# Kernel optimization log

Hardware: AMD Instinct MI355X
Metric: run time of the kernel (lower is better)

## Reference

```python
import jax, jax.numpy as jnp
import numpy as np

B, S, DIM, HEADS, DHEAD = 1, 1992, 2048, 16, 128
NKI_SEQ_ALIGN = 128
EPS = 1e-6


def setup_inputs() -> dict:
    key = jax.random.key(0)
    ks = jax.random.split(key, 8)
    hidden_states = jax.random.normal(ks[0], (B, S, DIM), dtype=jnp.float32)
    # realistic rotary tables, full head_dim with interleaved pair angles
    pos = jnp.arange(S, dtype=jnp.float32)
    inv_freq = 1.0 / (10000.0 ** (jnp.arange(0, DHEAD, 2, dtype=jnp.float32) / DHEAD))
    ang = pos[:, None] * inv_freq[None, :]                      # [S, DHEAD/2]
    full = jnp.stack([ang, ang], axis=-1).reshape(S, DHEAD)     # interleave
    freqs_cos = jnp.cos(full)[None, :, None, :]                 # [1,S,1,DHEAD]
    freqs_sin = jnp.sin(full)[None, :, None, :]
    sc = 0.02
    wq = jax.random.normal(ks[1], (DIM, DIM), dtype=jnp.float32) * sc
    wk = jax.random.normal(ks[2], (DIM, DIM), dtype=jnp.float32) * sc
    wv = jax.random.normal(ks[3], (DIM, DIM), dtype=jnp.float32) * sc
    wo = jax.random.normal(ks[4], (DIM, DIM), dtype=jnp.float32) * sc
    bq = jax.random.normal(ks[5], (DIM,), dtype=jnp.float32) * sc
    bk = jax.random.normal(ks[6], (DIM,), dtype=jnp.float32) * sc
    bv = jax.random.normal(ks[7], (DIM,), dtype=jnp.float32) * sc
    bo = jnp.zeros((DIM,), dtype=jnp.float32)
    norm_q_w = jnp.ones((DIM,), dtype=jnp.float32)
    norm_k_w = jnp.ones((DIM,), dtype=jnp.float32)
    return dict(hidden_states=hidden_states, freqs_cos=freqs_cos, freqs_sin=freqs_sin,
                wq=wq, bq=bq, wk=wk, bk=bk, wv=wv, bv=bv,
                norm_q_w=norm_q_w, norm_k_w=norm_k_w, wo=wo, bo=bo)


def _rms_norm(x, weight, eps=EPS):
    xf = x.astype(jnp.float32)
    var = jnp.mean(xf * xf, axis=-1, keepdims=True)
    return (weight * (xf * jax.lax.rsqrt(var + eps))).astype(x.dtype)


def _apply_rope(x, freqs_cos, freqs_sin):
    # x: [B,H,S,D]; freqs: [1,S,1,D]
    cos = jnp.transpose(freqs_cos[..., 0::2], (0, 2, 1, 3))  # [1,1,S,D/2]
    sin = jnp.transpose(freqs_sin[..., 1::2], (0, 2, 1, 3))
    x1, x2 = x[..., 0::2], x[..., 1::2]
    o1 = x1 * cos - x2 * sin
    o2 = x1 * sin + x2 * cos
    return jnp.stack([o1, o2], axis=-1).reshape(x.shape)


def _attention_padded(q, k, v):
    # Faithful to nki_flash_attention: zero-pad seq to multiple of 128,
    # no masking of padded keys (they contribute logit 0), trim query pad.
    B_, H_, S_, D_ = q.shape
    pad = (-S_) % NKI_SEQ_ALIGN
    if pad:
        pc = [(0, 0), (0, 0), (0, pad), (0, 0)]
        q = jnp.pad(q, pc); k = jnp.pad(k, pc); v = jnp.pad(v, pc)
    scale = 1.0 / np.sqrt(D_)
    scores = jnp.einsum('bhqd,bhkd->bhqk', q, k) * scale
    probs = jax.nn.softmax(scores, axis=-1)
    out = jnp.einsum('bhqk,bhkd->bhqd', probs, v)
    return out[:, :, :S_, :]


def reference(hidden_states, freqs_cos, freqs_sin, wq, bq, wk, bk, wv, bv,
              norm_q_w, norm_k_w, wo, bo):
    b, s, _ = hidden_states.shape
    q = hidden_states @ wq.T + bq
    k = hidden_states @ wk.T + bk
    v = hidden_states @ wv.T + bv
    q = _rms_norm(q, norm_q_w)
    k = _rms_norm(k, norm_k_w)
    hd = q.shape[-1] // HEADS
    q = q.reshape(b, s, HEADS, hd).transpose(0, 2, 1, 3)
    k = k.reshape(b, s, HEADS, hd).transpose(0, 2, 1, 3)
    v = v.reshape(b, s, HEADS, hd).transpose(0, 2, 1, 3)
    q = _apply_rope(q, freqs_cos, freqs_sin)
    k = _apply_rope(k, freqs_cos, freqs_sin)
    o = _attention_padded(q, k, v)
    o = o.transpose(0, 2, 1, 3).reshape(b, s, -1)
    return o @ wo.T + bo
```

## Files before the change

### kernel.cpp

```cpp
#include <hip/hip_runtime.h>
#include <cstdint>

#define S_REAL 1992
#define S_PAD  2048
#define DIMSZ  2048
#define NHEAD  16
#define DHD    128

typedef float f32x4 __attribute__((ext_vector_type(4)));
typedef float f32x16 __attribute__((ext_vector_type(16)));
typedef __bf16 bf16x8 __attribute__((ext_vector_type(8)));
typedef unsigned short u16x8 __attribute__((ext_vector_type(8)));

__device__ __forceinline__ unsigned short f2bf(float f){
  uint32_t u = __float_as_uint(f);
  u += 0x7fffu + ((u >> 16) & 1u);
  return (unsigned short)(u >> 16);
}

__device__ __forceinline__ void gload16(const void* g, void* l){
  __builtin_amdgcn_global_load_lds(
      (const __attribute__((address_space(1))) uint32_t*)g,
      (__attribute__((address_space(3))) uint32_t*)l,
      16, 0, 0);
}

template<int N> __device__ __forceinline__ void waitbar(){
  if constexpr (N == 4) asm volatile("s_waitcnt vmcnt(4)\n\ts_barrier" ::: "memory");
  else                  asm volatile("s_waitcnt vmcnt(0)\n\ts_barrier" ::: "memory");
}

__launch_bounds__(256)
__global__ void k_cvt5(const float* __restrict__ s0, const float* __restrict__ s1,
                       const float* __restrict__ s2, const float* __restrict__ s3,
                       const float* __restrict__ s4,
                       unsigned short* __restrict__ d0, unsigned short* __restrict__ d1,
                       unsigned short* __restrict__ d2, unsigned short* __restrict__ d3,
                       unsigned short* __restrict__ d4,
                       int nX, int nW)
{
  int i = blockIdx.x * 256 + threadIdx.x;
  const float* s; unsigned short* d; int j;
  if (i < nX){ s = s0; d = d0; j = i; }
  else {
    int k = i - nX;
    int wsel = k / nW; j = k - wsel * nW;
    s = (wsel == 0) ? s1 : (wsel == 1) ? s2 : (wsel == 2) ? s3 : s4;
    d = (wsel == 0) ? d1 : (wsel == 1) ? d2 : (wsel == 2) ? d3 : d4;
  }
  const float4* sp = (const float4*)s + (size_t)j * 2;
  float4 a = sp[0], b = sp[1];
  u16x8 o;
  o[0]=f2bf(a.x); o[1]=f2bf(a.y); o[2]=f2bf(a.z); o[3]=f2bf(a.w);
  o[4]=f2bf(b.x); o[5]=f2bf(b.y); o[6]=f2bf(b.z); o[7]=f2bf(b.w);
  *((u16x8*)d + j) = o;
}

__launch_bounds__(256, 3)
__global__ void k_g32(const unsigned short* __restrict__ A,
                      const unsigned short* __restrict__ B0,
                      const unsigned short* __restrict__ B1,
                      const unsigned short* __restrict__ B2,
                      const float* __restrict__ bias0,
                      const float* __restrict__ bias1,
                      const float* __restrict__ bias2,
                      float* __restrict__ C0, float* __restrict__ C1,
                      unsigned short* __restrict__ Cb,
                      int Mreal)
{
  constexpr int BUFE = 8192;
  constexpr int NT   = DIMSZ / 32;
  __shared__ unsigned short lds[3 * BUFE];

  const unsigned short* Bm = (blockIdx.z == 0) ? B0 : ((blockIdx.z == 1) ? B1 : B2);
  const float* bias        = (blockIdx.z == 0) ? bias0 : ((blockIdx.z == 1) ? bias1 : bias2);
  float* C                 = (blockIdx.z == 0) ? C0 : C1;

  const int fid = blockIdx.x + gridDim.x * blockIdx.y;
  const int q   = (gridDim.x * gridDim.y) >> 3;
  const int nf  = (fid & 7) * q + (fid >> 3);
  const int m0  = (nf >> 4) * 128, n0 = (nf & 15) * 128;

  const int tid = threadIdx.x;
  const int w = tid >> 6, l = tid & 63;
  const int l31 = l & 31, l5 = l >> 5;
  const int wr = (w >> 1) * 64, wc = (w & 1) * 64;

  f32x16 acc[2][2];
  #pragma unroll
  for (int mb = 0; mb < 2; ++mb)
    #pragma unroll
    for (int nb = 0; nb < 2; ++nb)
      #pragma unroll
      for (int r = 0; r < 16; ++r) acc[mb][nb][r] = 0.f;

#define G32_STAGE(TT, BASE) do{                                                   \
    const int k0s = (TT) * 32;                                                    \
    unsigned short* dst = (BASE);                                                 \
    _Pragma("unroll")                                                             \
    for (int i_ = 0; i_ < 2; ++i_){                                               \
      int lin = i_ * 256 + tid;                                                   \
      int r_ = lin >> 2, pos_ = lin & 3;                                          \
      int gr_ = m0 + r_; if (gr_ > Mreal - 1) gr_ = Mreal - 1;                    \
      gload16(A + (size_t)gr_ * DIMSZ + k0s + (pos_ ^ ((r_ >> 1) & 3)) * 8,       \
              dst + lin * 8);                                                     \
    }                                                                             \
    _Pragma("unroll")                                                             \
    for (int i_ = 0; i_ < 2; ++i_){                                               \
      int lin = i_ * 256 + tid;                                                   \
      int r_ = lin >> 2, pos_ = lin & 3;                                          \
      gload16(Bm + (size_t)(n0 + r_) * DIMSZ + k0s + (pos_ ^ ((r_ >> 1) & 3)) * 8,\
              dst + 4096 + lin * 8);                                              \
    }                                                                             \
  } while(0)

#define G32_COMPUTE(BASE) do{                                                     \
    const unsigned short* sb = (BASE);                                            \
    bf16x8 a_[2][2], b_[2][2];                                                    \
    _Pragma("unroll")                                                             \
    for (int mb = 0; mb < 2; ++mb)                                                \
      _Pragma("unroll")                                                           \
      for (int ks = 0; ks < 2; ++ks){                                             \
        int r_ = wr + mb * 32 + l31;                                              \
        int c_ = (ks * 2 + l5) ^ ((r_ >> 1) & 3);                                 \
        a_[mb][ks] = *(const bf16x8*)(sb + r_ * 32 + c_ * 8);                     \
      }                                                                           \
    _Pragma("unroll")                                                             \
    for (int nb = 0; nb < 2; ++nb)                                                \
      _Pragma("unroll")                                                           \
      for (int ks = 0; ks < 2; ++ks){                                             \
        int r_ = wc + nb * 32 + l31;                                              \
        int c_ = (ks * 2 + l5) ^ ((r_ >> 1) & 3);                                 \
        b_[nb][ks] = *(const bf16x8*)(sb + 4096 + r_ * 32 + c_ * 8);              \
      }                                                                           \
    __builtin_amdgcn_s_setprio(1);                                                \
    _Pragma("unroll")                                                             \
    for (int ks = 0; ks < 2; ++ks)                                                \
      _Pragma("unroll")                                                           \
      for (int mb = 0; mb < 2; ++mb)                                              \
        _Pragma("unroll")                                                         \
        for (int nb = 0; nb < 2; ++nb)                                            \
          acc[mb][nb] = __builtin_amdgcn_mfma_f32_32x32x16_bf16(a_[mb][ks],       \
                            b_[nb][ks], acc[mb][nb], 0, 0, 0);                    \
    __builtin_amdgcn_s_setprio(0);                                                \
  } while(0)

  G32_STAGE(0, lds);
  G32_STAGE(1, lds + BUFE);
  int bc = 0, bs = 2;
  for (int tt = 0; tt < NT - 2; ++tt){
    waitbar<4>();
    G32_STAGE(tt + 2, lds + bs * BUFE);
    G32_COMPUTE(lds + bc * BUFE);
    bs = (bs == 2) ? 0 : bs + 1;
    bc = (bc == 2) ? 0 : bc + 1;
  }
  waitbar<4>();
  G32_COMPUTE(lds + bc * BUFE);
  bc = (bc == 2) ? 0 : bc + 1;
  waitbar<0>();
  G32_COMPUTE(lds + bc * BUFE);

#undef G32_STAGE
#undef G32_COMPUTE

  const bool vout = (blockIdx.z == 2);
  #pragma unroll
  for (int nb = 0; nb < 2; ++nb){
    int col = n0 + wc + nb * 32 + l31;
    float bz = bias[col];
    #pragma unroll
    for (int mb = 0; mb < 2; ++mb){
      #pragma unroll
      for (int r = 0; r < 16; ++r){
        int row = m0 + wr + mb * 32 + (r & 3) + 8 * (r >> 2) + 4 * l5;
        if (row < Mreal){
          if (vout) Cb[(size_t)row * DIMSZ + col] = f2bf(acc[mb][nb][r] + bz);
          else      C[(size_t)row * DIMSZ + col] = acc[mb][nb][r] + bz;
        }
      }
    }
  }
}

__launch_bounds__(256)
__global__ void k_normrope2(const float* __restrict__ Qf, const float* __restrict__ Kf,
                            const float* __restrict__ nqw, const float* __restrict__ nkw,
                            const float* __restrict__ fc, const float* __restrict__ fs,
                            unsigned short* __restrict__ OutQ, unsigned short* __restrict__ OutK)
{
  const int s = blockIdx.x;
  const int isK = blockIdx.y;
  const float* Xf = isK ? Kf : Qf;
  const float* nw = isK ? nkw : nqw;
  unsigned short* Out = isK ? OutK : OutQ;
  const float scale = isK ? 1.0f : 0.08838834764831843f;
  const int swz = isK;

  const int t = threadIdx.x;
  const int w = t >> 6, l = t & 63;
  __shared__ float wred[4];
  float v[8];
  float ss = 0.f;
  if (s < S_REAL){
    const float4* p = (const float4*)(Xf + (size_t)s * DIMSZ) + t * 2;
    float4 a = p[0], b = p[1];
    v[0]=a.x; v[1]=a.y; v[2]=a.z; v[3]=a.w; v[4]=b.x; v[5]=b.y; v[6]=b.z; v[7]=b.w;
    #pragma unroll
    for (int j = 0; j < 8; ++j) ss += v[j] * v[j];
  }
  #pragma unroll
  for (int off = 32; off >= 1; off >>= 1) ss += __shfl_xor(ss, off);
  if (l == 0) wred[w] = ss;
  __syncthreads();
  float tot = wred[0] + wred[1] + wred[2] + wred[3];
  float rinv = rsqrtf(tot * (1.f / DIMSZ) + 1e-6f);

  const int h  = t >> 4;
  const int d0 = (t & 15) * 8;
  const int b  = t & 15;
  const int bsw = swz ? (b ^ (s & 7)) : b;
  unsigned short* dst = Out + ((size_t)h * S_PAD + s) * DHD + bsw * 8;
  u16x8 o;
  if (s < S_REAL){
    #pragma unroll
    for (int i = 0; i < 4; ++i){
      float c_ = fc[s * DHD + d0 + 2 * i];
      float s_ = fs[s * DHD + d0 + 2 * i + 1];
      float x1 = v[2 * i]     * rinv * nw[t * 8 + 2 * i];
      float x2 = v[2 * i + 1] * rinv * nw[t * 8 + 2 * i + 1];
      o[2 * i]     = f2bf((x1 * c_ - x2 * s_) * scale);
      o[2 * i + 1] = f2bf((x1 * s_ + x2 * c_) * scale);
    }
  } else {
    #pragma unroll
    for (int j = 0; j < 8; ++j) o[j] = 0;
  }
  *(u16x8*)dst = o;
}

__launch_bounds__(256)
__global__ void k_vtrans(const unsigned short* __restrict__ Vb, unsigned short* __restrict__ Vth)
{
  __shared__ unsigned short tile[64][72];
  const int t = threadIdx.x;
  const int s0 = blockIdx.x * 64, c0 = blockIdx.y * 64;
  #pragma unroll
  for (int i = 0; i < 2; ++i){
    int lin = i * 256 + t;
    int r = lin >> 3, ck = lin & 7;
    u16x8 val = (u16x8){0,0,0,0,0,0,0,0};
    if (s0 + r < S_REAL)
      val = *(const u16x8*)(Vb + (size_t)(s0 + r) * DIMSZ + c0 + ck * 8);
    *(u16x8*)&tile[r][ck * 8] = val;
  }
  __syncthreads();
  const int cl = t >> 2;
  const int cc = c0 + cl;
  #pragma unroll
  for (int bi = 0; bi < 2; ++bi){
    int b = (t & 3) * 2 + bi;
    u16x8 o;
    #pragma unroll
    for (int j = 0; j < 8; ++j) o[j] = tile[b * 8 + j][cl];
    int bsw = b ^ (cc & 7);
    *(u16x8*)(Vth + (size_t)cc * S_PAD + s0 + bsw * 8) = o;
  }
}

__launch_bounds__(512)
__global__ void k_attn(const unsigned short* __restrict__ Qh,
                       const unsigned short* __restrict__ Kh,
                       const unsigned short* __restrict__ Vth,
                       unsigned short* __restrict__ O)
{
  __shared__ unsigned short kbuf[3][64 * 128];
  __shared__ unsigned short vbuf[3][128 * 64];
  __shared__ unsigned short pbuf[8][16 * 64];
  const int h = blockIdx.y;
  const int q0 = blockIdx.x * 128;
  const int t = threadIdx.x, w = t >> 6, l = t & 63;
  const int lr = l & 15, lg = l >> 4;

  const unsigned short* Qp = Qh + ((size_t)h * S_PAD + q0 + w * 16 + lr) * DHD;
  bf16x8 qf[4];
  #pragma unroll
  for (int ks = 0; ks < 4; ++ks) qf[ks] = *(const bf16x8*)(Qp + ks * 32 + lg * 8);

  f32x4 acc[8];
  #pragma unroll
  for (int nf = 0; nf < 8; ++nf) acc[nf] = (f32x4){0.f, 0.f, 0.f, 0.f};
  float m = -3.0e38f, lsum = 0.f;

#define ATT_STAGE(KT, BI) do{                                                       \
    _Pragma("unroll")                                                               \
    for (int i_ = 0; i_ < 2; ++i_){                                                 \
      int lin = i_ * 512 + t;                                                       \
      int rK = lin >> 4, ckK = lin & 15;                                            \
      gload16(Kh + ((size_t)h * S_PAD + (KT) * 64 + rK) * DHD + ckK * 8,            \
              &kbuf[BI][lin * 8]);                                                  \
    }                                                                               \
    _Pragma("unroll")                                                               \
    for (int i_ = 0; i_ < 2; ++i_){                                                 \
      int lin = i_ * 512 + t;                                                       \
      int rV = lin >> 3, ckV = lin & 7;                                             \
      gload16(Vth + ((size_t)h * DHD + rV) * S_PAD + (KT) * 64 + ckV * 8,           \
              &vbuf[BI][lin * 8]);                                                  \
    }                                                                               \
  } while(0)

  ATT_STAGE(0, 0);
  ATT_STAGE(1, 1);
  asm volatile("s_waitcnt vmcnt(4)" ::: "memory");
  __builtin_amdgcn_s_barrier();

  constexpr int NKT = S_PAD / 64;
  for (int kt = 0; kt < NKT; ++kt){
    const int bi = kt % 3;
    if (kt < NKT - 2) ATT_STAGE(kt + 2, (kt + 2) % 3);

    f32x4 sf[4];
    __builtin_amdgcn_s_setprio(1);
    #pragma unroll
    for (int kvf = 0; kvf < 4; ++kvf){
      sf[kvf] = (f32x4){0.f, 0.f, 0.f, 0.f};
      int r = kvf * 16 + lr;
      #pragma unroll
      for (int ks = 0; ks < 4; ++ks){
        int blk = (ks * 4 + lg) ^ (r & 7);
        bf16x8 kf = *(const bf16x8*)&kbuf[bi][r * 128 + blk * 8];
        sf[kvf] = __builtin_amdgcn_mfma_f32_16x16x32_bf16(kf, qf[ks], sf[kvf], 0, 0, 0);
      }
    }
    __builtin_amdgcn_s_setprio(0);

    float pmax = sf[0][0];
    #pragma unroll
    for (int kvf = 0; kvf < 4; ++kvf)
      #pragma unroll
      for (int j = 0; j < 4; ++j) pmax = fmaxf(pmax, sf[kvf][j]);
    pmax = fmaxf(pmax, __shfl_xor(pmax, 16));
    pmax = fmaxf(pmax, __shfl_xor(pmax, 32));

    float fr = 1.f;
    if (!__all(pmax - m <= 8.0f)){
      float mn = fmaxf(m, pmax);
      fr = __expf(m - mn);
      m = mn;
      float fv0 = __shfl(fr, lg * 4 + 0);
      float fv1 = __shfl(fr, lg * 4 + 1);
      float fv2 = __shfl(fr, lg * 4 + 2);
      float fv3 = __shfl(fr, lg * 4 + 3);
      f32x4 fv = (f32x4){fv0, fv1, fv2, fv3};
      #pragma unroll
      for (int nf = 0; nf < 8; ++nf) acc[nf] *= fv;
    }

    float p[4][4];
    float psum = 0.f;
    #pragma unroll
    for (int kvf = 0; kvf < 4; ++kvf)
      #pragma unroll
      for (int j = 0; j < 4; ++j){ p[kvf][j] = __expf(sf[kvf][j] - m); psum += p[kvf][j]; }
    lsum = lsum * fr + psum;

    char* pb = (char*)pbuf[w];
    #pragma unroll
    for (int kvf = 0; kvf < 4; ++kvf){
      uint2 wv;
      wv.x = (uint32_t)f2bf(p[kvf][0]) | ((uint32_t)f2bf(p[kvf][1]) << 16);
      wv.y = (uint32_t)f2bf(p[kvf][2]) | ((uint32_t)f2bf(p[kvf][3]) << 16);
      int byte = lr * 128 + (((kvf * 2 + (lg >> 1)) ^ (lr & 7)) * 16) + (lg & 1) * 8;
      *(uint2*)(pb + byte) = wv;
    }
    bf16x8 pf[2];
    #pragma unroll
    for (int c = 0; c < 2; ++c)
      pf[c] = *(const bf16x8*)(pb + lr * 128 + ((c * 4 + lg) ^ (lr & 7)) * 16);

    __builtin_amdgcn_s_setprio(1);
    #pragma unroll
    for (int nf = 0; nf < 8; ++nf){
      int cc = nf * 16 + lr;
      #pragma unroll
      for (int ks = 0; ks < 2; ++ks){
        int blk = (ks * 4 + lg) ^ (cc & 7);
        bf16x8 vf = *(const bf16x8*)&vbuf[bi][cc * 64 + blk * 8];
        acc[nf] = __builtin_amdgcn_mfma_f32_16x16x32_bf16(pf[ks], vf, acc[nf], 0, 0, 0);
      }
    }
    __builtin_amdgcn_s_setprio(0);

    if (kt < NKT - 2)       asm volatile("s_waitcnt vmcnt(4)" ::: "memory");
    else if (kt == NKT - 2) asm volatile("s_waitcnt vmcnt(0)" ::: "memory");
    if (kt < NKT - 1) __builtin_amdgcn_s_barrier();
  }
#undef ATT_STAGE

  lsum += __shfl_xor(lsum, 16);
  lsum += __shfl_xor(lsum, 32);
  float ls0 = __shfl(lsum, lg * 4 + 0);
  float ls1 = __shfl(lsum, lg * 4 + 1);
  float ls2 = __shfl(lsum, lg * 4 + 2);
  float ls3 = __shfl(lsum, lg * 4 + 3);
  f32x4 lsv = (f32x4){1.f / ls0, 1.f / ls1, 1.f / ls2, 1.f / ls3};

  #pragma unroll
  for (int nf = 0; nf < 8; ++nf){
    #pragma unroll
    for (int j = 0; j < 4; ++j){
      int row = q0 + w * 16 + lg * 4 + j;
      if (row < S_REAL)
        O[(size_t)row * DIMSZ + h * DHD + nf * 16 + lr] = f2bf(acc[nf][j] * lsv[j]);
    }
  }
}

extern "C" void kernel_launch(void* const* d_in, const int* in_sizes, int n_in,
                              void* d_out, int out_size, void* d_ws, size_t ws_size,
                              hipStream_t stream)
{
  const float* hidden = (const float*)d_in[0];
  const float* fc  = (const float*)d_in[1];
  const float* fs  = (const float*)d_in[2];
  const float* wq  = (const float*)d_in[3];
  const float* bq  = (const float*)d_in[4];
  const float* wk  = (const float*)d_in[5];
  const float* bk  = (const float*)d_in[6];
  const float* wv  = (const float*)d_in[7];
  const float* bv  = (const float*)d_in[8];
  const float* nqw = (const float*)d_in[9];
  const float* nkw = (const float*)d_in[10];
  const float* wo  = (const float*)d_in[11];
  const float* bo  = (const float*)d_in[12];
  float* out = (float*)d_out;

  char* ws = (char*)d_ws;
  size_t off = 0;
  auto alloc = [&](size_t bytes) -> void* {
    void* p = ws + off;
    off += (bytes + 255) & ~(size_t)255;
    return p;
  };
  unsigned short* Xb  = (unsigned short*)alloc((size_t)S_REAL * DIMSZ * 2);
  unsigned short* Wqb = (unsigned short*)alloc((size_t)DIMSZ * DIMSZ * 2);
  unsigned short* Wkb = (unsigned short*)alloc((size_t)DIMSZ * DIMSZ * 2);
  unsigned short* Wvb = (unsigned short*)alloc((size_t)DIMSZ * DIMSZ * 2);
  unsigned short* Wob = (unsigned short*)alloc((size_t)DIMSZ * DIMSZ * 2);
  float* Qf = (float*)alloc((size_t)S_REAL * DIMSZ * 4);
  float* Kf = (float*)alloc((size_t)S_REAL * DIMSZ * 4);
  unsigned short* Vb  = (unsigned short*)alloc((size_t)S_REAL * DIMSZ * 2);
  unsigned short* Qhh = (unsigned short*)alloc((size_t)NHEAD * S_PAD * DHD * 2);
  unsigned short* Khh = (unsigned short*)alloc((size_t)NHEAD * S_PAD * DHD * 2);
  unsigned short* Vth = (unsigned short*)alloc((size_t)NHEAD * DHD * S_PAD * 2);
  unsigned short* Oa  = (unsigned short*)alloc((size_t)S_REAL * DIMSZ * 2);

  {
    int nX = S_REAL * DIMSZ / 8;
    int nW = DIMSZ * DIMSZ / 8;
    int total = nX + 4 * nW;
    k_cvt5<<<total / 256, 256, 0, stream>>>(hidden, wq, wk, wv, wo,
                                            Xb, Wqb, Wkb, Wvb, Wob, nX, nW);
  }

  k_g32<<<dim3(16, 16, 3), 256, 0, stream>>>(Xb, Wqb, Wkb, Wvb, bq, bk, bv,
                                             Qf, Kf, Vb, S_REAL);

  k_normrope2<<<dim3(S_PAD, 2), 256, 0, stream>>>(Qf, Kf, nqw, nkw, fc, fs, Qhh, Khh);

  k_vtrans<<<dim3(S_PAD / 64, DIMSZ / 64), 256, 0, stream>>>(Vb, Vth);

  k_attn<<<dim3(S_PAD / 128, NHEAD), 512, 0, stream>>>(Qhh, Khh, Vth, Oa);

  k_g32<<<dim3(16, 16, 1), 256, 0, stream>>>(Oa, Wob, Wob, Wob, bo, bo, bo,
                                             out, out, nullptr, S_REAL);
}
```

Measured before the change: 221.2 us.

## Deepen GEMM K-tile, software-pipeline attention softmax, use exp2 and head swizzle

```diff
diff --git a/kernel.cpp b/kernel.cpp
--- a/kernel.cpp
+++ b/kernel.cpp
@@ -23,11 +23,6 @@
       (const __attribute__((address_space(1))) uint32_t*)g,
       (__attribute__((address_space(3))) uint32_t*)l,
       16, 0, 0);
-}
-
-template<int N> __device__ __forceinline__ void waitbar(){
-  if constexpr (N == 4) asm volatile("s_waitcnt vmcnt(4)\n\ts_barrier" ::: "memory");
-  else                  asm volatile("s_waitcnt vmcnt(0)\n\ts_barrier" ::: "memory");
 }
 
 __launch_bounds__(256)
@@ -56,8 +51,9 @@
   *((u16x8*)d + j) = o;
 }
 
-__launch_bounds__(256, 3)
-__global__ void k_g32(const unsigned short* __restrict__ A,
+template<int BN>
+__launch_bounds__(256, 2)
+__global__ void k_g64(const unsigned short* __restrict__ A,
                       const unsigned short* __restrict__ B0,
                       const unsigned short* __restrict__ B1,
                       const unsigned short* __restrict__ B2,
@@ -68,9 +64,16 @@
                       unsigned short* __restrict__ Cb,
                       int Mreal)
 {
-  constexpr int BUFE = 8192;
-  constexpr int NT   = DIMSZ / 32;
-  __shared__ unsigned short lds[3 * BUFE];
+  constexpr int WN   = (BN == 128) ? 2 : 1;
+  constexpr int WM   = 4 / WN;
+  constexpr int MB   = (128 / WM) / 32;
+  constexpr int NB   = (BN / WN) / 32;
+  constexpr int AE   = 128 * 64;
+  constexpr int BE   = BN * 64;
+  constexpr int BUFE = AE + BE;
+  constexpr int NT   = DIMSZ / 64;
+  constexpr int TN   = DIMSZ / BN;
+  __shared__ unsigned short lds[2 * BUFE];
 
   const unsigned short* Bm = (blockIdx.z == 0) ? B0 : ((blockIdx.z == 1) ? B1 : B2);
   const float* bias        = (blockIdx.z == 0) ? bias0 : ((blockIdx.z == 1) ? bias1 : bias2);
@@ -79,98 +82,94 @@
   const int fid = blockIdx.x + gridDim.x * blockIdx.y;
   const int q   = (gridDim.x * gridDim.y) >> 3;
   const int nf  = (fid & 7) * q + (fid >> 3);
-  const int m0  = (nf >> 4) * 128, n0 = (nf & 15) * 128;
+  const int m0  = (nf / TN) * 128, n0 = (nf % TN) * BN;
 
   const int tid = threadIdx.x;
   const int w = tid >> 6, l = tid & 63;
   const int l31 = l & 31, l5 = l >> 5;
-  const int wr = (w >> 1) * 64, wc = (w & 1) * 64;
-
-  f32x16 acc[2][2];
-  #pragma unroll
-  for (int mb = 0; mb < 2; ++mb)
-    #pragma unroll
-    for (int nb = 0; nb < 2; ++nb)
+  const int wr = (w / WN) * (128 / WM);
+  const int wc = (w % WN) * (BN / WN);
+
+  f32x16 acc[MB][NB];
+  #pragma unroll
+  for (int mb = 0; mb < MB; ++mb)
+    #pragma unroll
+    for (int nb = 0; nb < NB; ++nb)
       #pragma unroll
       for (int r = 0; r < 16; ++r) acc[mb][nb][r] = 0.f;
 
-#define G32_STAGE(TT, BASE) do{                                                   \
-    const int k0s = (TT) * 32;                                                    \
-    unsigned short* dst = (BASE);                                                 \
+#define G64_STAGE(TT, PP) do{                                                     \
+    const int k0s = (TT) * 64;                                                    \
+    unsigned short* dst = &lds[(PP) * BUFE];                                      \
     _Pragma("unroll")                                                             \
-    for (int i_ = 0; i_ < 2; ++i_){                                               \
+    for (int i_ = 0; i_ < AE / 2048; ++i_){                                       \
       int lin = i_ * 256 + tid;                                                   \
-      int r_ = lin >> 2, pos_ = lin & 3;                                          \
+      int r_ = lin >> 3, sl_ = lin & 7;                                           \
       int gr_ = m0 + r_; if (gr_ > Mreal - 1) gr_ = Mreal - 1;                    \
-      gload16(A + (size_t)gr_ * DIMSZ + k0s + (pos_ ^ ((r_ >> 1) & 3)) * 8,       \
+      gload16(A + (size_t)gr_ * DIMSZ + k0s + (sl_ ^ (r_ & 7)) * 8,               \
               dst + lin * 8);                                                     \
     }                                                                             \
     _Pragma("unroll")                                                             \
-    for (int i_ = 0; i_ < 2; ++i_){                                               \
+    for (int i_ = 0; i_ < BE / 2048; ++i_){                                       \
       int lin = i_ * 256 + tid;                                                   \
-      int r_ = lin >> 2, pos_ = lin & 3;                                          \
-      gload16(Bm + (size_t)(n0 + r_) * DIMSZ + k0s + (pos_ ^ ((r_ >> 1) & 3)) * 8,\
-              dst + 4096 + lin * 8);                                              \
+      int r_ = lin >> 3, sl_ = lin & 7;                                           \
+      gload16(Bm + (size_t)(n0 + r_) * DIMSZ + k0s + (sl_ ^ (r_ & 7)) * 8,        \
+              dst + AE + lin * 8);                                                \
     }                                                                             \
   } while(0)
 
-#define G32_COMPUTE(BASE) do{                                                     \
-    const unsigned short* sb = (BASE);                                            \
-    bf16x8 a_[2][2], b_[2][2];                                                    \
+#define G64_COMPUTE(PP) do{                                                       \
+    const unsigned short* sb = &lds[(PP) * BUFE];                                 \
+    bf16x8 a_[MB][4], b_[NB][4];                                                  \
     _Pragma("unroll")                                                             \
-    for (int mb = 0; mb < 2; ++mb)                                                \
+    for (int mb = 0; mb < MB; ++mb)                                               \
       _Pragma("unroll")                                                           \
-      for (int ks = 0; ks < 2; ++ks){                                             \
+      for (int ks = 0; ks < 4; ++ks){                                             \
         int r_ = wr + mb * 32 + l31;                                              \
-        int c_ = (ks * 2 + l5) ^ ((r_ >> 1) & 3);                                 \
-        a_[mb][ks] = *(const bf16x8*)(sb + r_ * 32 + c_ * 8);                     \
+        int c_ = (ks * 2 + l5) ^ (r_ & 7);                                        \
+        a_[mb][ks] = *(const bf16x8*)(sb + r_ * 64 + c_ * 8);                     \
       }                                                                           \
     _Pragma("unroll")                                                             \
-    for (int nb = 0; nb < 2; ++nb)                                                \
+    for (int nb = 0; nb < NB; ++nb)                                               \
       _Pragma("unroll")                                                           \
-      for (int ks = 0; ks < 2; ++ks){                                             \
+      for (int ks = 0; ks < 4; ++ks){                                             \
         int r_ = wc + nb * 32 + l31;                                              \
-        int c_ = (ks * 2 + l5) ^ ((r_ >> 1) & 3);                                 \
-        b_[nb][ks] = *(const bf16x8*)(sb + 4096 + r_ * 32 + c_ * 8);              \
+        int c_ = (ks * 2 + l5) ^ (r_ & 7);                                        \
+        b_[nb][ks] = *(const bf16x8*)(sb + AE + r_ * 64 + c_ * 8);                \
       }                                                                           \
     __builtin_amdgcn_s_setprio(1);                                                \
     _Pragma("unroll")                                                             \
-    for (int ks = 0; ks < 2; ++ks)                                                \
+    for (int ks = 0; ks < 4; ++ks)                                                \
       _Pragma("unroll")                                                           \
-      for (int mb = 0; mb < 2; ++mb)                                              \
+      for (int mb = 0; mb < MB; ++mb)                                             \
         _Pragma("unroll")                                                         \
-        for (int nb = 0; nb < 2; ++nb)                                            \
+        for (int nb = 0; nb < NB; ++nb)                                           \
           acc[mb][nb] = __builtin_amdgcn_mfma_f32_32x32x16_bf16(a_[mb][ks],       \
                             b_[nb][ks], acc[mb][nb], 0, 0, 0);                    \
     __builtin_amdgcn_s_setprio(0);                                                \
   } while(0)
 
-  G32_STAGE(0, lds);
-  G32_STAGE(1, lds + BUFE);
-  int bc = 0, bs = 2;
-  for (int tt = 0; tt < NT - 2; ++tt){
-    waitbar<4>();
-    G32_STAGE(tt + 2, lds + bs * BUFE);
-    G32_COMPUTE(lds + bc * BUFE);
-    bs = (bs == 2) ? 0 : bs + 1;
-    bc = (bc == 2) ? 0 : bc + 1;
-  }
-  waitbar<4>();
-  G32_COMPUTE(lds + bc * BUFE);
-  bc = (bc == 2) ? 0 : bc + 1;
-  waitbar<0>();
-  G32_COMPUTE(lds + bc * BUFE);
-
-#undef G32_STAGE
-#undef G32_COMPUTE
+  G64_STAGE(0, 0);
+  asm volatile("s_waitcnt vmcnt(0)" ::: "memory");
+  __builtin_amdgcn_s_barrier();
+  int p = 0;
+  for (int tt = 0; tt < NT; ++tt){
+    if (tt + 1 < NT) G64_STAGE(tt + 1, p ^ 1);
+    G64_COMPUTE(p);
+    asm volatile("s_waitcnt vmcnt(0)" ::: "memory");
+    __builtin_amdgcn_s_barrier();
+    p ^= 1;
+  }
+#undef G64_STAGE
+#undef G64_COMPUTE
 
   const bool vout = (blockIdx.z == 2);
   #pragma unroll
-  for (int nb = 0; nb < 2; ++nb){
+  for (int nb = 0; nb < NB; ++nb){
     int col = n0 + wc + nb * 32 + l31;
     float bz = bias[col];
     #pragma unroll
-    for (int mb = 0; mb < 2; ++mb){
+    for (int mb = 0; mb < MB; ++mb){
       #pragma unroll
       for (int r = 0; r < 16; ++r){
         int row = m0 + wr + mb * 32 + (r & 3) + 8 * (r >> 2) + 4 * l5;
@@ -194,7 +193,7 @@
   const float* Xf = isK ? Kf : Qf;
   const float* nw = isK ? nkw : nqw;
   unsigned short* Out = isK ? OutK : OutQ;
-  const float scale = isK ? 1.0f : 0.08838834764831843f;
+  const float scale = isK ? 1.0f : (0.08838834764831843f * 1.4426950408889634f);
   const int swz = isK;
 
   const int t = threadIdx.x;
@@ -275,10 +274,11 @@
                        unsigned short* __restrict__ O)
 {
   __shared__ unsigned short kbuf[3][64 * 128];
-  __shared__ unsigned short vbuf[3][128 * 64];
+  __shared__ unsigned short vbuf[4][128 * 64];
   __shared__ unsigned short pbuf[8][16 * 64];
-  const int h = blockIdx.y;
-  const int q0 = blockIdx.x * 128;
+  const int flat = blockIdx.x + gridDim.x * blockIdx.y;
+  const int h  = (flat & 7) * 2 + ((flat >> 3) & 1);
+  const int q0 = (flat >> 4) * 128;
   const int t = threadIdx.x, w = t >> 6, l = t & 63;
   const int lr = l & 15, lg = l >> 4;
 
@@ -292,110 +292,121 @@
   for (int nf = 0; nf < 8; ++nf) acc[nf] = (f32x4){0.f, 0.f, 0.f, 0.f};
   float m = -3.0e38f, lsum = 0.f;
 
-#define ATT_STAGE(KT, BI) do{                                                       \
+#define ATT_STAGE(KT, BK_, BV_) do{                                                 \
     _Pragma("unroll")                                                               \
     for (int i_ = 0; i_ < 2; ++i_){                                                 \
       int lin = i_ * 512 + t;                                                       \
       int rK = lin >> 4, ckK = lin & 15;                                            \
       gload16(Kh + ((size_t)h * S_PAD + (KT) * 64 + rK) * DHD + ckK * 8,            \
-              &kbuf[BI][lin * 8]);                                                  \
+              &kbuf[BK_][lin * 8]);                                                 \
     }                                                                               \
     _Pragma("unroll")                                                               \
     for (int i_ = 0; i_ < 2; ++i_){                                                 \
       int lin = i_ * 512 + t;                                                       \
       int rV = lin >> 3, ckV = lin & 7;                                             \
       gload16(Vth + ((size_t)h * DHD + rV) * S_PAD + (KT) * 64 + ckV * 8,           \
-              &vbuf[BI][lin * 8]);                                                  \
+              &vbuf[BV_][lin * 8]);                                                 \
     }                                                                               \
   } while(0)
 
-  ATT_STAGE(0, 0);
-  ATT_STAGE(1, 1);
+#define SM_PV(SF, VB) do{                                                           \
+    float pmax = SF[0][0];                                                          \
+    _Pragma("unroll")                                                               \
+    for (int kvf = 0; kvf < 4; ++kvf)                                               \
+      _Pragma("unroll")                                                             \
+      for (int j = 0; j < 4; ++j) pmax = fmaxf(pmax, SF[kvf][j]);                   \
+    pmax = fmaxf(pmax, __shfl_xor(pmax, 16));                                       \
+    pmax = fmaxf(pmax, __shfl_xor(pmax, 32));                                       \
+    float fr = 1.f;                                                                 \
+    if (!__all(pmax - m <= 8.0f)){                                                  \
+      float mn = fmaxf(m, pmax);                                                    \
+      fr = exp2f(m - mn);                                                           \
+      m = mn;                                                                       \
+      float fv0 = __shfl(fr, lg * 4 + 0);                                           \
+      float fv1 = __shfl(fr, lg * 4 + 1);                                           \
+      float fv2 = __shfl(fr, lg * 4 + 2);                                           \
+      float fv3 = __shfl(fr, lg * 4 + 3);                                           \
+      f32x4 fv = (f32x4){fv0, fv1, fv2, fv3};                                       \
+      _Pragma("unroll")                                                             \
+      for (int nf = 0; nf < 8; ++nf) acc[nf] *= fv;                                 \
+    }                                                                               \
+    float p_[4][4];                                                                 \
+    float psum = 0.f;                                                               \
+    _Pragma("unroll")                                                               \
+    for (int kvf = 0; kvf < 4; ++kvf)                                               \
+      _Pragma("unroll")                                                             \
+      for (int j = 0; j < 4; ++j){ p_[kvf][j] = exp2f(SF[kvf][j] - m); psum += p_[kvf][j]; } \
+    lsum = lsum * fr + psum;                                                        \
+    char* pb = (char*)pbuf[w];                                                      \
+    _Pragma("unroll")                                                               \
+    for (int kvf = 0; kvf < 4; ++kvf){                                              \
+      uint2 wv;                                                                     \
+      wv.x = (uint32_t)f2bf(p_[kvf][0]) | ((uint32_t)f2bf(p_[kvf][1]) << 16);       \
+      wv.y = (uint32_t)f2bf(p_[kvf][2]) | ((uint32_t)f2bf(p_[kvf][3]) << 16);       \
+      int byte = lr * 128 + (((kvf * 2 + (lg >> 1)) ^ (lr & 7)) * 16) + (lg & 1) * 8;\
+      *(uint2*)(pb + byte) = wv;                                                    \
+    }                                                                               \
+    bf16x8 pf[2];                                                                   \
+    _Pragma("unroll")                                                               \
+    for (int c = 0; c < 2; ++c)                                                     \
+      pf[c] = *(const bf16x8*)(pb + lr * 128 + ((c * 4 + lg) ^ (lr & 7)) * 16);     \
+    __builtin_amdgcn_s_setprio(1);                                                  \
+    _Pragma("unroll")                                                               \
+    for (int nf = 0; nf < 8; ++nf){                                                 \
+      int cc = nf * 16 + lr;                                                        \
+      _Pragma("unroll")                                                             \
+      for (int ks = 0; ks < 2; ++ks){                                               \
+        int blk = (ks * 4 + lg) ^ (cc & 7);                                         \
+        bf16x8 vf = *(const bf16x8*)&vbuf[VB][cc * 64 + blk * 8];                   \
+        acc[nf] = __builtin_amdgcn_mfma_f32_16x16x32_bf16(pf[ks], vf, acc[nf], 0, 0, 0); \
+      }                                                                             \
+    }                                                                               \
+    __builtin_amdgcn_s_setprio(0);                                                  \
+  } while(0)
+
+  ATT_STAGE(0, 0, 0);
+  ATT_STAGE(1, 1, 1);
   asm volatile("s_waitcnt vmcnt(4)" ::: "memory");
   __builtin_amdgcn_s_barrier();
 
   constexpr int NKT = S_PAD / 64;
+  f32x4 sfp[4];
+  int kb = 0, sk = 2, sv = 2, vp = 3;
   for (int kt = 0; kt < NKT; ++kt){
-    const int bi = kt % 3;
-    if (kt < NKT - 2) ATT_STAGE(kt + 2, (kt + 2) % 3);
-
-    f32x4 sf[4];
+    if (kt < NKT - 2) ATT_STAGE(kt + 2, sk, sv);
+
+    f32x4 sfc[4];
     __builtin_amdgcn_s_setprio(1);
     #pragma unroll
     for (int kvf = 0; kvf < 4; ++kvf){
-      sf[kvf] = (f32x4){0.f, 0.f, 0.f, 0.f};
+      sfc[kvf] = (f32x4){0.f, 0.f, 0.f, 0.f};
       int r = kvf * 16 + lr;
       #pragma unroll
       for (int ks = 0; ks < 4; ++ks){
         int blk = (ks * 4 + lg) ^ (r & 7);
-        bf16x8 kf = *(const bf16x8*)&kbuf[bi][r * 128 + blk * 8];
-        sf[kvf] = __builtin_amdgcn_mfma_f32_16x16x32_bf16(kf, qf[ks], sf[kvf], 0, 0, 0);
+        bf16x8 kf = *(const bf16x8*)&kbuf[kb][r * 128 + blk * 8];
+        sfc[kvf] = __builtin_amdgcn_mfma_f32_16x16x32_bf16(kf, qf[ks], sfc[kvf], 0, 0, 0);
       }
     }
     __builtin_amdgcn_s_setprio(0);
 
-    float pmax = sf[0][0];
-    #pragma unroll
-    for (int kvf = 0; kvf < 4; ++kvf)
-      #pragma unroll
-      for (int j = 0; j < 4; ++j) pmax = fmaxf(pmax, sf[kvf][j]);
-    pmax = fmaxf(pmax, __shfl_xor(pmax, 16));
-    pmax = fmaxf(pmax, __shfl_xor(pmax, 32));
-
-    float fr = 1.f;
-    if (!__all(pmax - m <= 8.0f)){
-      float mn = fmaxf(m, pmax);
-      fr = __expf(m - mn);
-      m = mn;
-      float fv0 = __shfl(fr, lg * 4 + 0);
-      float fv1 = __shfl(fr, lg * 4 + 1);
-      float fv2 = __shfl(fr, lg * 4 + 2);
-      float fv3 = __shfl(fr, lg * 4 + 3);
-      f32x4 fv = (f32x4){fv0, fv1, fv2, fv3};
-      #pragma unroll
-      for (int nf = 0; nf < 8; ++nf) acc[nf] *= fv;
-    }
-
-    float p[4][4];
-    float psum = 0.f;
-    #pragma unroll
-    for (int kvf = 0; kvf < 4; ++kvf)
-      #pragma unroll
-      for (int j = 0; j < 4; ++j){ p[kvf][j] = __expf(sf[kvf][j] - m); psum += p[kvf][j]; }
-    lsum = lsum * fr + psum;
-
-    char* pb = (char*)pbuf[w];
-    #pragma unroll
-    for (int kvf = 0; kvf < 4; ++kvf){
-      uint2 wv;
-      wv.x = (uint32_t)f2bf(p[kvf][0]) | ((uint32_t)f2bf(p[kvf][1]) << 16);
-      wv.y = (uint32_t)f2bf(p[kvf][2]) | ((uint32_t)f2bf(p[kvf][3]) << 16);
-      int byte = lr * 128 + (((kvf * 2 + (lg >> 1)) ^ (lr & 7)) * 16) + (lg & 1) * 8;
-      *(uint2*)(pb + byte) = wv;
-    }
-    bf16x8 pf[2];
-    #pragma unroll
-    for (int c = 0; c < 2; ++c)
-      pf[c] = *(const bf16x8*)(pb + lr * 128 + ((c * 4 + lg) ^ (lr & 7)) * 16);
-
-    __builtin_amdgcn_s_setprio(1);
-    #pragma unroll
-    for (int nf = 0; nf < 8; ++nf){
-      int cc = nf * 16 + lr;
-      #pragma unroll
-      for (int ks = 0; ks < 2; ++ks){
-        int blk = (ks * 4 + lg) ^ (cc & 7);
-        bf16x8 vf = *(const bf16x8*)&vbuf[bi][cc * 64 + blk * 8];
-        acc[nf] = __builtin_amdgcn_mfma_f32_16x16x32_bf16(pf[ks], vf, acc[nf], 0, 0, 0);
-      }
-    }
-    __builtin_amdgcn_s_setprio(0);
+    if (kt > 0) SM_PV(sfp, vp);
+
+    #pragma unroll
+    for (int kvf = 0; kvf < 4; ++kvf) sfp[kvf] = sfc[kvf];
 
     if (kt < NKT - 2)       asm volatile("s_waitcnt vmcnt(4)" ::: "memory");
     else if (kt == NKT - 2) asm volatile("s_waitcnt vmcnt(0)" ::: "memory");
     if (kt < NKT - 1) __builtin_amdgcn_s_barrier();
-  }
+
+    kb = (kb == 2) ? 0 : kb + 1;
+    sk = (sk == 2) ? 0 : sk + 1;
+    sv = (sv == 3) ? 0 : sv + 1;
+    vp = (vp == 3) ? 0 : vp + 1;
+  }
+  SM_PV(sfp, vp);
 #undef ATT_STAGE
+#undef SM_PV
 
   lsum += __shfl_xor(lsum, 16);
   lsum += __shfl_xor(lsum, 32);
@@ -463,8 +474,8 @@
                                             Xb, Wqb, Wkb, Wvb, Wob, nX, nW);
   }
 
-  k_g32<<<dim3(16, 16, 3), 256, 0, stream>>>(Xb, Wqb, Wkb, Wvb, bq, bk, bv,
-                                             Qf, Kf, Vb, S_REAL);
+  k_g64<128><<<dim3(16, 16, 3), 256, 0, stream>>>(Xb, Wqb, Wkb, Wvb, bq, bk, bv,
+                                                  Qf, Kf, Vb, S_REAL);
 
   k_normrope2<<<dim3(S_PAD, 2), 256, 0, stream>>>(Qf, Kf, nqw, nkw, fc, fs, Qhh, Khh);
 
@@ -472,6 +483,6 @@
 
   k_attn<<<dim3(S_PAD / 128, NHEAD), 512, 0, stream>>>(Qhh, Khh, Vth, Oa);
 
-  k_g32<<<dim3(16, 16, 1), 256, 0, stream>>>(Oa, Wob, Wob, Wob, bo, bo, bo,
-                                             out, out, nullptr, S_REAL);
-}
+  k_g64<64><<<dim3(16, 32, 1), 256, 0, stream>>>(Oa, Wob, Wob, Wob, bo, bo, bo,
+                                                 out, out, nullptr, S_REAL);
+}
```

Result: slower. 233.8 us (+5.7%).
